# Kernel tuning notes

Hardware: AMD Instinct MI355X
Metric: run time of the kernel (lower is better)

Reference implementation:

```python
import jax, jax.numpy as jnp
import numpy as np

NUM_TAGS = 3


def setup_inputs() -> dict:
    key = jax.random.key(0)
    k1, k2, k3 = jax.random.split(key, 3)
    B, T, K = 2048, 4096, NUM_TAGS
    logits = jax.random.normal(k1, (B, T, K), dtype=jnp.float32)
    transitions = jax.random.normal(k2, (K, K), dtype=jnp.float32)
    tags = jax.random.randint(k3, (B, T), 0, K, dtype=jnp.int64)
    return {"logits": logits, "transitions": transitions, "tags": tags}


def reference(logits, transitions, tags):
    """Negative CRF log-likelihood (AllenNLP CRF, include_start_end_transitions=False,
    full mask), i.e. -(sum_b [joint_score(b) - log_partition(b)])."""
    # --- log partition via forward algorithm (lax.scan over time) ---
    # alpha: [B, K]; emissions scanned over time: [T-1, B, K]
    def step(alpha, emit_t):
        # broadcast: alpha[b, i] + transitions[i, j] -> logsumexp over i
        new_alpha = jax.nn.logsumexp(alpha[:, :, None] + transitions[None, :, :], axis=1) + emit_t
        return new_alpha, None

    alpha0 = logits[:, 0, :]                              # [B, K]
    emits_rest = jnp.swapaxes(logits[:, 1:, :], 0, 1)     # [T-1, B, K]
    alpha_T, _ = jax.lax.scan(step, alpha0, emits_rest)
    log_z = jax.nn.logsumexp(alpha_T, axis=1)             # [B]

    # --- joint (numerator) score of the gold tag sequence ---
    emit_score = jnp.take_along_axis(logits, tags[:, :, None], axis=2)[..., 0].sum(axis=1)  # [B]
    trans_score = transitions[tags[:, :-1], tags[:, 1:]].sum(axis=1)                         # [B]

    loglik = emit_score + trans_score - log_z
    return -jnp.sum(loglik)
```

## Files before the change

kernel.cpp:

```cpp
#include <hip/hip_runtime.h>

#define BB 2048
#define TT 4096
#define LN2 0.69314718055994530942f

template<int CTRL>
__device__ __forceinline__ float dppf(float x) {
    return __int_as_float(__builtin_amdgcn_update_dpp(
        0, __float_as_int(x), CTRL, 0xF, 0xF, true));
}
template<int CTRL>
__device__ __forceinline__ int dppi(int x) {
    return __builtin_amdgcn_update_dpp(0, x, CTRL, 0xF, 0xF, true);
}

__global__ __launch_bounds__(512) void crf_pass1(
    const float* __restrict__ logits, const float* __restrict__ trans,
    const int* __restrict__ tags, float* __restrict__ ws)
{
    __shared__ float sTrans[9];
    __shared__ float sTrExp[9];
    __shared__ float sRec[7][12];
    __shared__ float sV[3];
    const int tid = threadIdx.x;
    if (tid < 9) {
        float tv = trans[tid];
        sTrans[tid] = tv;
        sTrExp[tid] = __expf(tv);
    }
    __syncthreads();

    const int b = blockIdx.x;
    const int c = tid;

    const int4*   tp = (const int4*)(tags + (size_t)b * TT + (size_t)c * 8);
    const float4* lp = (const float4*)(logits + ((size_t)b * TT + (size_t)c * 8) * 3);

    int4 Tq0 = tp[0], Tq1 = tp[1];
    float Lf[24];
#pragma unroll
    for (int i = 0; i < 6; ++i) {
        float4 t = lp[i];
        Lf[4*i+0] = t.x; Lf[4*i+1] = t.y; Lf[4*i+2] = t.z; Lf[4*i+3] = t.w;
    }
    __builtin_amdgcn_sched_barrier(0);

    unsigned pk =  (unsigned)Tq0.x        | ((unsigned)Tq0.y << 2)
                | ((unsigned)Tq0.z << 4)  | ((unsigned)Tq0.w << 6)
                | ((unsigned)Tq1.x << 8)  | ((unsigned)Tq1.y << 10)
                | ((unsigned)Tq1.z << 12) | ((unsigned)Tq1.w << 14);

    const float t00 = sTrExp[0], t01 = sTrExp[1], t02 = sTrExp[2];
    const float t10 = sTrExp[3], t11 = sTrExp[4], t12 = sTrExp[5];
    const float t20 = sTrExp[6], t21 = sTrExp[7], t22 = sTrExp[8];

    float a00 = 1.f, a01 = 0.f, a02 = 0.f;
    float a10 = 0.f, a11 = 1.f, a12 = 0.f;
    float a20 = 0.f, a21 = 0.f, a22 = 1.f;
    int   se = 0;
    float score = 0.f;
    unsigned acc = 0u;
    int prev = 0;
    float v0 = 0.f, v1 = 0.f, v2 = 0.f;

#define MATSTEP(e0_, e1_, e2_) do {                                     \
    float x0 = __expf(e0_), x1 = __expf(e1_), x2 = __expf(e2_);         \
    float b0_ = (a00*t00 + a01*t10 + a02*t20) * x0;                     \
    float b1_ = (a00*t01 + a01*t11 + a02*t21) * x1;                     \
    float b2_ = (a00*t02 + a01*t12 + a02*t22) * x2;                     \
    float b3_ = (a10*t00 + a11*t10 + a12*t20) * x0;                     \
    float b4_ = (a10*t01 + a11*t11 + a12*t21) * x1;                     \
    float b5_ = (a10*t02 + a11*t12 + a12*t22) * x2;                     \
    float b6_ = (a20*t00 + a21*t10 + a22*t20) * x0;                     \
    float b7_ = (a20*t01 + a21*t11 + a22*t21) * x1;                     \
    float b8_ = (a20*t02 + a21*t12 + a22*t22) * x2;                     \
    a00=b0_; a01=b1_; a02=b2_; a10=b3_; a11=b4_; a12=b5_; a20=b6_; a21=b7_; a22=b8_; \
} while (0)

#define RENORM do {                                                     \
    float m_ = fmaxf(fmaxf(fmaxf(a00, a01), fmaxf(a02, a10)),           \
                     fmaxf(fmaxf(a11, a12), fmaxf(fmaxf(a20, a21), a22))); \
    int ef_ = (int)(__float_as_uint(m_) >> 23);                         \
    float scf_ = __uint_as_float((unsigned)(254 - ef_) << 23);          \
    se += ef_ - 127;                                                    \
    a00 *= scf_; a01 *= scf_; a02 *= scf_;                              \
    a10 *= scf_; a11 *= scf_; a12 *= scf_;                              \
    a20 *= scf_; a21 *= scf_; a22 *= scf_;                              \
} while (0)

#pragma unroll
    for (int s = 0; s < 8; ++s) {
        float e0 = Lf[3*s+0], e1 = Lf[3*s+1], e2 = Lf[3*s+2];
        int tg = (int)((pk >> (2*s)) & 3u);
        if (s == 0) {
            if (c == 0) {
                v0 = __expf(e0); v1 = __expf(e1); v2 = __expf(e2);
            } else {
                MATSTEP(e0, e1, e2);
            }
        } else {
            MATSTEP(e0, e1, e2);
            acc += 1u << (3 * (prev * 3 + tg));
        }
        score += (tg == 0) ? e0 : ((tg == 1) ? e1 : e2);
        prev = tg;
    }
    RENORM;

#pragma unroll
    for (int p = 0; p < 9; ++p)
        score += (float)((int)((acc >> (3 * p)) & 7u)) * sTrans[p];

    const int lane = tid & 63;
    const int wid  = tid >> 6;

    {
        int opv = __shfl_up(prev, 1, 64);
        if (lane != 0) score += sTrans[opv * 3 + (int)(pk & 3u)];
    }

    int fp = (int)(pk & 3u) | (prev << 8);

#define FOLD_ROUND(CTRL) do {                                           \
    float o00=dppf<CTRL>(a00), o01=dppf<CTRL>(a01), o02=dppf<CTRL>(a02);\
    float o10=dppf<CTRL>(a10), o11=dppf<CTRL>(a11), o12=dppf<CTRL>(a12);\
    float o20=dppf<CTRL>(a20), o21=dppf<CTRL>(a21), o22=dppf<CTRL>(a22);\
    int   ose=dppi<CTRL>(se);                                           \
    float osc=dppf<CTRL>(score);                                        \
    int   ofp=dppi<CTRL>(fp);                                           \
    float c00=o00*a00+o01*a10+o02*a20;                                  \
    float c01=o00*a01+o01*a11+o02*a21;                                  \
    float c02=o00*a02+o01*a12+o02*a22;                                  \
    float c10=o10*a00+o11*a10+o12*a20;                                  \
    float c11=o10*a01+o11*a11+o12*a21;                                  \
    float c12=o10*a02+o11*a12+o12*a22;                                  \
    float c20=o20*a00+o21*a10+o22*a20;                                  \
    float c21=o20*a01+o21*a11+o22*a21;                                  \
    float c22=o20*a02+o21*a12+o22*a22;                                  \
    score += osc; se += ose;                                            \
    fp = (ofp & 255) | (fp & 0xFF00);                                   \
    a00=c00; a01=c01; a02=c02; a10=c10; a11=c11; a12=c12;               \
    a20=c20; a21=c21; a22=c22;                                          \
    RENORM;                                                             \
} while (0)

    FOLD_ROUND(0x111);
    FOLD_ROUND(0x112);
    FOLD_ROUND(0x114);
    FOLD_ROUND(0x118);
    FOLD_ROUND(0x142);
    FOLD_ROUND(0x143);

    if (lane == 63 && wid < 7) {
        sRec[wid][0] = a00; sRec[wid][1] = a01; sRec[wid][2] = a02;
        sRec[wid][3] = a10; sRec[wid][4] = a11; sRec[wid][5] = a12;
        sRec[wid][6] = a20; sRec[wid][7] = a21; sRec[wid][8] = a22;
        sRec[wid][9]  = __int_as_float(se);
        sRec[wid][10] = score;
        sRec[wid][11] = __int_as_float(fp);
    }
    if (tid == 0) { sV[0] = v0; sV[1] = v1; sV[2] = v2; }
    __syncthreads();

    if (tid == 511) {
        float p00 = sRec[0][0], p01 = sRec[0][1], p02 = sRec[0][2];
        float p10 = sRec[0][3], p11 = sRec[0][4], p12 = sRec[0][5];
        float p20 = sRec[0][6], p21 = sRec[0][7], p22 = sRec[0][8];
        int   seT   = __float_as_int(sRec[0][9]);
        float scT   = sRec[0][10];
        int   lastT = __float_as_int(sRec[0][11]) >> 8;

#define RENORMP do {                                                    \
    float m_ = fmaxf(fmaxf(fmaxf(p00, p01), fmaxf(p02, p10)),           \
                     fmaxf(fmaxf(p11, p12), fmaxf(fmaxf(p20, p21), p22))); \
    int ef_ = (int)(__float_as_uint(m_) >> 23);                         \
    float scf_ = __uint_as_float((unsigned)(254 - ef_) << 23);          \
    seT += ef_ - 127;                                                   \
    p00 *= scf_; p01 *= scf_; p02 *= scf_;                              \
    p10 *= scf_; p11 *= scf_; p12 *= scf_;                              \
    p20 *= scf_; p21 *= scf_; p22 *= scf_;                              \
} while (0)

#pragma unroll
        for (int k = 1; k < 7; ++k) {
            float m00 = sRec[k][0], m01 = sRec[k][1], m02 = sRec[k][2];
            float m10 = sRec[k][3], m11 = sRec[k][4], m12 = sRec[k][5];
            float m20 = sRec[k][6], m21 = sRec[k][7], m22 = sRec[k][8];
            int   shm = __float_as_int(sRec[k][9]);
            float scm = sRec[k][10];
            int   pkm = __float_as_int(sRec[k][11]);

            float c00 = p00*m00 + p01*m10 + p02*m20;
            float c01 = p00*m01 + p01*m11 + p02*m21;
            float c02 = p00*m02 + p01*m12 + p02*m22;
            float c10 = p10*m00 + p11*m10 + p12*m20;
            float c11 = p10*m01 + p11*m11 + p12*m21;
            float c12 = p10*m02 + p11*m12 + p12*m22;
            float c20 = p20*m00 + p21*m10 + p22*m20;
            float c21 = p20*m01 + p21*m11 + p22*m21;
            float c22 = p20*m02 + p21*m12 + p22*m22;

            scT += scm + sTrans[lastT * 3 + (pkm & 255)];
            lastT = pkm >> 8;
            seT  += shm;
            p00=c00; p01=c01; p02=c02; p10=c10; p11=c11; p12=c12;
            p20=c20; p21=c21; p22=c22;
            RENORMP;
        }
        {
            float c00 = p00*a00 + p01*a10 + p02*a20;
            float c01 = p00*a01 + p01*a11 + p02*a21;
            float c02 = p00*a02 + p01*a12 + p02*a22;
            float c10 = p10*a00 + p11*a10 + p12*a20;
            float c11 = p10*a01 + p11*a11 + p12*a21;
            float c12 = p10*a02 + p11*a12 + p12*a22;
            float c20 = p20*a00 + p21*a10 + p22*a20;
            float c21 = p20*a01 + p21*a11 + p22*a21;
            float c22 = p20*a02 + p21*a12 + p22*a22;

            scT += score + sTrans[lastT * 3 + (fp & 255)];
            seT += se;
            p00=c00; p01=c01; p02=c02; p10=c10; p11=c11; p12=c12;
            p20=c20; p21=c21; p22=c22;
        }
        float w0 = sV[0], w1 = sV[1], w2 = sV[2];
        float n0 = w0*p00 + w1*p10 + w2*p20;
        float n1 = w0*p01 + w1*p11 + w2*p21;
        float n2 = w0*p02 + w1*p12 + w2*p22;
        float logz = logf(n0 + n1 + n2) + (float)seT * LN2;
        ws[b] = logz - scT;
#undef RENORMP
    }

#undef MATSTEP
#undef RENORM
#undef FOLD_ROUND
}

__global__ __launch_bounds__(256) void crf_reduce(
    const float* __restrict__ ws, float* __restrict__ out)
{
    int tid = threadIdx.x;
    float s = 0.f;
#pragma unroll
    for (int k = 0; k < BB / 256; ++k) s += ws[k * 256 + tid];
    for (int off = 32; off > 0; off >>= 1) s += __shfl_down(s, off, 64);
    __shared__ float sP[4];
    if ((tid & 63) == 0) sP[tid >> 6] = s;
    __syncthreads();
    if (tid == 0) out[0] = sP[0] + sP[1] + sP[2] + sP[3];
}

extern "C" void kernel_launch(void* const* d_in, const int* in_sizes, int n_in,
                              void* d_out, int out_size, void* d_ws, size_t ws_size,
                              hipStream_t stream) {
    const float* logits = (const float*)d_in[0];
    const float* trans  = (const float*)d_in[1];
    const int*   tags   = (const int*)d_in[2];
    float* out = (float*)d_out;
    float* ws  = (float*)d_ws;

    crf_pass1<<<dim3(BB), dim3(512), 0, stream>>>(logits, trans, tags, ws);
    crf_reduce<<<dim3(1), dim3(256), 0, stream>>>(ws, out);
}
```

Measured before the change: 32.59 us.

## Process two batch rows per block with next-row loads overlapping the fold

Each block now handles two sequences instead of one, halving the grid. The loads of the next row's tags and logits are issued before the DPP fold and block-level combine of the current row, so memory latency overlaps with the reduction work. This costs extra registers and adds a second barrier per row, and with fewer blocks there is less parallelism across CUs.

```diff
diff --git a/kernel.cpp b/kernel.cpp
--- a/kernel.cpp
+++ b/kernel.cpp
@@ -3,6 +3,7 @@
 #define BB 2048
 #define TT 4096
 #define LN2 0.69314718055994530942f
+#define ROWS 2
 
 template<int CTRL>
 __device__ __forceinline__ float dppf(float x) {
@@ -30,38 +31,29 @@
     }
     __syncthreads();
 
-    const int b = blockIdx.x;
-    const int c = tid;
-
-    const int4*   tp = (const int4*)(tags + (size_t)b * TT + (size_t)c * 8);
-    const float4* lp = (const float4*)(logits + ((size_t)b * TT + (size_t)c * 8) * 3);
-
-    int4 Tq0 = tp[0], Tq1 = tp[1];
+    const int c    = tid;
+    const int b0   = blockIdx.x * ROWS;
+    const int lane = tid & 63;
+    const int wid  = tid >> 6;
+
+    int4  Tq0, Tq1;
     float Lf[24];
-#pragma unroll
-    for (int i = 0; i < 6; ++i) {
-        float4 t = lp[i];
-        Lf[4*i+0] = t.x; Lf[4*i+1] = t.y; Lf[4*i+2] = t.z; Lf[4*i+3] = t.w;
+    {
+        const int4*   tp = (const int4*)(tags + (size_t)b0 * TT + (size_t)c * 8);
+        const float4* lp = (const float4*)(logits + ((size_t)b0 * TT + (size_t)c * 8) * 3);
+        Tq0 = tp[0]; Tq1 = tp[1];
+#pragma unroll
+        for (int i = 0; i < 6; ++i) {
+            float4 t = lp[i];
+            Lf[4*i+0] = t.x; Lf[4*i+1] = t.y; Lf[4*i+2] = t.z; Lf[4*i+3] = t.w;
+        }
     }
     __builtin_amdgcn_sched_barrier(0);
 
-    unsigned pk =  (unsigned)Tq0.x        | ((unsigned)Tq0.y << 2)
-                | ((unsigned)Tq0.z << 4)  | ((unsigned)Tq0.w << 6)
-                | ((unsigned)Tq1.x << 8)  | ((unsigned)Tq1.y << 10)
-                | ((unsigned)Tq1.z << 12) | ((unsigned)Tq1.w << 14);
-
-    const float t00 = sTrExp[0], t01 = sTrExp[1], t02 = sTrExp[2];
-    const float t10 = sTrExp[3], t11 = sTrExp[4], t12 = sTrExp[5];
-    const float t20 = sTrExp[6], t21 = sTrExp[7], t22 = sTrExp[8];
-
-    float a00 = 1.f, a01 = 0.f, a02 = 0.f;
-    float a10 = 0.f, a11 = 1.f, a12 = 0.f;
-    float a20 = 0.f, a21 = 0.f, a22 = 1.f;
-    int   se = 0;
-    float score = 0.f;
-    unsigned acc = 0u;
-    int prev = 0;
-    float v0 = 0.f, v1 = 0.f, v2 = 0.f;
+#define PACK(T0_, T1_) ( (unsigned)(T0_).x        | ((unsigned)(T0_).y << 2)  \
+                       | ((unsigned)(T0_).z << 4)  | ((unsigned)(T0_).w << 6)  \
+                       | ((unsigned)(T1_).x << 8)  | ((unsigned)(T1_).y << 10) \
+                       | ((unsigned)(T1_).z << 12) | ((unsigned)(T1_).w << 14) )
 
 #define MATSTEP(e0_, e1_, e2_) do {                                     \
     float x0 = __expf(e0_), x1 = __expf(e1_), x2 = __expf(e2_);         \
@@ -87,39 +79,6 @@
     a10 *= scf_; a11 *= scf_; a12 *= scf_;                              \
     a20 *= scf_; a21 *= scf_; a22 *= scf_;                              \
 } while (0)
-
-#pragma unroll
-    for (int s = 0; s < 8; ++s) {
-        float e0 = Lf[3*s+0], e1 = Lf[3*s+1], e2 = Lf[3*s+2];
-        int tg = (int)((pk >> (2*s)) & 3u);
-        if (s == 0) {
-            if (c == 0) {
-                v0 = __expf(e0); v1 = __expf(e1); v2 = __expf(e2);
-            } else {
-                MATSTEP(e0, e1, e2);
-            }
-        } else {
-            MATSTEP(e0, e1, e2);
-            acc += 1u << (3 * (prev * 3 + tg));
-        }
-        score += (tg == 0) ? e0 : ((tg == 1) ? e1 : e2);
-        prev = tg;
-    }
-    RENORM;
-
-#pragma unroll
-    for (int p = 0; p < 9; ++p)
-        score += (float)((int)((acc >> (3 * p)) & 7u)) * sTrans[p];
-
-    const int lane = tid & 63;
-    const int wid  = tid >> 6;
-
-    {
-        int opv = __shfl_up(prev, 1, 64);
-        if (lane != 0) score += sTrans[opv * 3 + (int)(pk & 3u)];
-    }
-
-    int fp = (int)(pk & 3u) | (prev << 8);
 
 #define FOLD_ROUND(CTRL) do {                                           \
     float o00=dppf<CTRL>(a00), o01=dppf<CTRL>(a01), o02=dppf<CTRL>(a02);\
@@ -144,31 +103,97 @@
     RENORM;                                                             \
 } while (0)
 
-    FOLD_ROUND(0x111);
-    FOLD_ROUND(0x112);
-    FOLD_ROUND(0x114);
-    FOLD_ROUND(0x118);
-    FOLD_ROUND(0x142);
-    FOLD_ROUND(0x143);
-
-    if (lane == 63 && wid < 7) {
-        sRec[wid][0] = a00; sRec[wid][1] = a01; sRec[wid][2] = a02;
-        sRec[wid][3] = a10; sRec[wid][4] = a11; sRec[wid][5] = a12;
-        sRec[wid][6] = a20; sRec[wid][7] = a21; sRec[wid][8] = a22;
-        sRec[wid][9]  = __int_as_float(se);
-        sRec[wid][10] = score;
-        sRec[wid][11] = __int_as_float(fp);
-    }
-    if (tid == 0) { sV[0] = v0; sV[1] = v1; sV[2] = v2; }
-    __syncthreads();
-
-    if (tid == 511) {
-        float p00 = sRec[0][0], p01 = sRec[0][1], p02 = sRec[0][2];
-        float p10 = sRec[0][3], p11 = sRec[0][4], p12 = sRec[0][5];
-        float p20 = sRec[0][6], p21 = sRec[0][7], p22 = sRec[0][8];
-        int   seT   = __float_as_int(sRec[0][9]);
-        float scT   = sRec[0][10];
-        int   lastT = __float_as_int(sRec[0][11]) >> 8;
+    unsigned pkCur = PACK(Tq0, Tq1);
+
+#pragma unroll
+    for (int r = 0; r < ROWS; ++r) {
+        const int b = b0 + r;
+        const unsigned pk = pkCur;
+
+        if (r + 1 < ROWS) {
+            const int4* tp2 = (const int4*)(tags + (size_t)(b + 1) * TT + (size_t)c * 8);
+            Tq0 = tp2[0]; Tq1 = tp2[1];
+        }
+
+        const float t00 = sTrExp[0], t01 = sTrExp[1], t02 = sTrExp[2];
+        const float t10 = sTrExp[3], t11 = sTrExp[4], t12 = sTrExp[5];
+        const float t20 = sTrExp[6], t21 = sTrExp[7], t22 = sTrExp[8];
+
+        float a00 = 1.f, a01 = 0.f, a02 = 0.f;
+        float a10 = 0.f, a11 = 1.f, a12 = 0.f;
+        float a20 = 0.f, a21 = 0.f, a22 = 1.f;
+        int   se = 0;
+        float score = 0.f;
+        unsigned acc = 0u;
+        int prev = 0;
+        float v0 = 0.f, v1 = 0.f, v2 = 0.f;
+
+#pragma unroll
+        for (int s = 0; s < 8; ++s) {
+            float e0 = Lf[3*s+0], e1 = Lf[3*s+1], e2 = Lf[3*s+2];
+            int tg = (int)((pk >> (2*s)) & 3u);
+            if (s == 0) {
+                if (c == 0) {
+                    v0 = __expf(e0); v1 = __expf(e1); v2 = __expf(e2);
+                } else {
+                    MATSTEP(e0, e1, e2);
+                }
+            } else {
+                MATSTEP(e0, e1, e2);
+                acc += 1u << (3 * (prev * 3 + tg));
+            }
+            score += (tg == 0) ? e0 : ((tg == 1) ? e1 : e2);
+            prev = tg;
+        }
+        RENORM;
+
+#pragma unroll
+        for (int p = 0; p < 9; ++p)
+            score += (float)((int)((acc >> (3 * p)) & 7u)) * sTrans[p];
+
+        if (c == 0) { sV[0] = v0; sV[1] = v1; sV[2] = v2; }
+
+        if (r + 1 < ROWS) {
+            pkCur = PACK(Tq0, Tq1);
+            const float4* lp2 = (const float4*)(logits + ((size_t)(b + 1) * TT + (size_t)c * 8) * 3);
+#pragma unroll
+            for (int i = 0; i < 6; ++i) {
+                float4 t = lp2[i];
+                Lf[4*i+0] = t.x; Lf[4*i+1] = t.y; Lf[4*i+2] = t.z; Lf[4*i+3] = t.w;
+            }
+        }
+        __builtin_amdgcn_sched_barrier(0);
+
+        {
+            int opv = __shfl_up(prev, 1, 64);
+            if (lane != 0) score += sTrans[opv * 3 + (int)(pk & 3u)];
+        }
+        int fp = (int)(pk & 3u) | (prev << 8);
+
+        FOLD_ROUND(0x111);
+        FOLD_ROUND(0x112);
+        FOLD_ROUND(0x114);
+        FOLD_ROUND(0x118);
+        FOLD_ROUND(0x142);
+        FOLD_ROUND(0x143);
+
+        if (lane == 63 && wid < 7) {
+            sRec[wid][0] = a00; sRec[wid][1] = a01; sRec[wid][2] = a02;
+            sRec[wid][3] = a10; sRec[wid][4] = a11; sRec[wid][5] = a12;
+            sRec[wid][6] = a20; sRec[wid][7] = a21; sRec[wid][8] = a22;
+            sRec[wid][9]  = __int_as_float(se);
+            sRec[wid][10] = score;
+            sRec[wid][11] = __int_as_float(fp);
+        }
+        __syncthreads();
+
+        if (tid == 511) {
+            float p00 = sRec[0][0], p01 = sRec[0][1], p02 = sRec[0][2];
+            float p10 = sRec[0][3], p11 = sRec[0][4], p12 = sRec[0][5];
+            float p20 = sRec[0][6], p21 = sRec[0][7], p22 = sRec[0][8];
+            int   seT   = __float_as_int(sRec[0][9]);
+            float scT   = sRec[0][10];
+            int   lastT = __float_as_int(sRec[0][11]) >> 8;
 
 #define RENORMP do {                                                    \
     float m_ = fmaxf(fmaxf(fmaxf(p00, p01), fmaxf(p02, p10)),           \
@@ -182,59 +207,62 @@
 } while (0)
 
 #pragma unroll
-        for (int k = 1; k < 7; ++k) {
-            float m00 = sRec[k][0], m01 = sRec[k][1], m02 = sRec[k][2];
-            float m10 = sRec[k][3], m11 = sRec[k][4], m12 = sRec[k][5];
-            float m20 = sRec[k][6], m21 = sRec[k][7], m22 = sRec[k][8];
-            int   shm = __float_as_int(sRec[k][9]);
-            float scm = sRec[k][10];
-            int   pkm = __float_as_int(sRec[k][11]);
-
-            float c00 = p00*m00 + p01*m10 + p02*m20;
-            float c01 = p00*m01 + p01*m11 + p02*m21;
-            float c02 = p00*m02 + p01*m12 + p02*m22;
-            float c10 = p10*m00 + p11*m10 + p12*m20;
-            float c11 = p10*m01 + p11*m11 + p12*m21;
-            float c12 = p10*m02 + p11*m12 + p12*m22;
-            float c20 = p20*m00 + p21*m10 + p22*m20;
-            float c21 = p20*m01 + p21*m11 + p22*m21;
-            float c22 = p20*m02 + p21*m12 + p22*m22;
-
-            scT += scm + sTrans[lastT * 3 + (pkm & 255)];
-            lastT = pkm >> 8;
-            seT  += shm;
-            p00=c00; p01=c01; p02=c02; p10=c10; p11=c11; p12=c12;
-            p20=c20; p21=c21; p22=c22;
-            RENORMP;
-        }
-        {
-            float c00 = p00*a00 + p01*a10 + p02*a20;
-            float c01 = p00*a01 + p01*a11 + p02*a21;
-            float c02 = p00*a02 + p01*a12 + p02*a22;
-            float c10 = p10*a00 + p11*a10 + p12*a20;
-            float c11 = p10*a01 + p11*a11 + p12*a21;
-            float c12 = p10*a02 + p11*a12 + p12*a22;
-            float c20 = p20*a00 + p21*a10 + p22*a20;
-            float c21 = p20*a01 + p21*a11 + p22*a21;
-            float c22 = p20*a02 + p21*a12 + p22*a22;
-
-            scT += score + sTrans[lastT * 3 + (fp & 255)];
-            seT += se;
-            p00=c00; p01=c01; p02=c02; p10=c10; p11=c11; p12=c12;
-            p20=c20; p21=c21; p22=c22;
-        }
-        float w0 = sV[0], w1 = sV[1], w2 = sV[2];
-        float n0 = w0*p00 + w1*p10 + w2*p20;
-        float n1 = w0*p01 + w1*p11 + w2*p21;
-        float n2 = w0*p02 + w1*p12 + w2*p22;
-        float logz = logf(n0 + n1 + n2) + (float)seT * LN2;
-        ws[b] = logz - scT;
+            for (int k = 1; k < 7; ++k) {
+                float m00 = sRec[k][0], m01 = sRec[k][1], m02 = sRec[k][2];
+                float m10 = sRec[k][3], m11 = sRec[k][4], m12 = sRec[k][5];
+                float m20 = sRec[k][6], m21 = sRec[k][7], m22 = sRec[k][8];
+                int   shm = __float_as_int(sRec[k][9]);
+                float scm = sRec[k][10];
+                int   pkm = __float_as_int(sRec[k][11]);
+
+                float c00 = p00*m00 + p01*m10 + p02*m20;
+                float c01 = p00*m01 + p01*m11 + p02*m21;
+                float c02 = p00*m02 + p01*m12 + p02*m22;
+                float c10 = p10*m00 + p11*m10 + p12*m20;
+                float c11 = p10*m01 + p11*m11 + p12*m21;
+                float c12 = p10*m02 + p11*m12 + p12*m22;
+                float c20 = p20*m00 + p21*m10 + p22*m20;
+                float c21 = p20*m01 + p21*m11 + p22*m21;
+                float c22 = p20*m02 + p21*m12 + p22*m22;
+
+                scT += scm + sTrans[lastT * 3 + (pkm & 255)];
+                lastT = pkm >> 8;
+                seT  += shm;
+                p00=c00; p01=c01; p02=c02; p10=c10; p11=c11; p12=c12;
+                p20=c20; p21=c21; p22=c22;
+                RENORMP;
+            }
+            {
+                float c00 = p00*a00 + p01*a10 + p02*a20;
+                float c01 = p00*a01 + p01*a11 + p02*a21;
+                float c02 = p00*a02 + p01*a12 + p02*a22;
+                float c10 = p10*a00 + p11*a10 + p12*a20;
+                float c11 = p10*a01 + p11*a11 + p12*a21;
+                float c12 = p10*a02 + p11*a12 + p12*a22;
+                float c20 = p20*a00 + p21*a10 + p22*a20;
+                float c21 = p20*a01 + p21*a11 + p22*a21;
+                float c22 = p20*a02 + p21*a12 + p22*a22;
+
+                scT += score + sTrans[lastT * 3 + (fp & 255)];
+                seT += se;
+                p00=c00; p01=c01; p02=c02; p10=c10; p11=c11; p12=c12;
+                p20=c20; p21=c21; p22=c22;
+            }
+            float w0 = sV[0], w1 = sV[1], w2 = sV[2];
+            float n0 = w0*p00 + w1*p10 + w2*p20;
+            float n1 = w0*p01 + w1*p11 + w2*p21;
+            float n2 = w0*p02 + w1*p12 + w2*p22;
+            float logz = logf(n0 + n1 + n2) + (float)seT * LN2;
+            ws[b] = logz - scT;
 #undef RENORMP
+        }
+        if (r + 1 < ROWS) __syncthreads();
     }
 
 #undef MATSTEP
 #undef RENORM
 #undef FOLD_ROUND
+#undef PACK
 }
 
 __global__ __launch_bounds__(256) void crf_reduce(
@@ -260,6 +288,6 @@
     float* out = (float*)d_out;
     float* ws  = (float*)d_ws;
 
-    crf_pass1<<<dim3(BB), dim3(512), 0, stream>>>(logits, trans, tags, ws);
+    crf_pass1<<<dim3(BB / ROWS), dim3(512), 0, stream>>>(logits, trans, tags, ws);
     crf_reduce<<<dim3(1), dim3(256), 0, stream>>>(ws, out);
 }
```

Measured after the change: 38.64 us. +18.6%, slower.
